# Kernel optimization log

Hardware: AMD Instinct MI355X
Metric: run time of the kernel (lower is better)

Reference implementation:

```python
import jax, jax.numpy as jnp
import numpy as np

B, N, H = 8, 1024, 1024
HEADS, DH = 16, 64  # H = HEADS * DH
LN_EPS = 1e-12


def setup_inputs() -> dict:
    key = jax.random.key(0)
    ks = jax.random.split(key, 8)
    s = 0.02
    return {
        "hidden_states": jax.random.normal(ks[0], (B, N, H), jnp.float32),
        "role_mask": jax.random.randint(ks[1], (B, N, N), 0, 2, jnp.int32),
        "conv_len": jax.random.randint(ks[2], (B,), 0, 160, jnp.int32),
        "Wq": jax.random.normal(ks[3], (H, H), jnp.float32) * s,
        "bq": jnp.zeros((H,), jnp.float32),
        "Wk": jax.random.normal(ks[4], (H, H), jnp.float32) * s,
        "bk": jnp.zeros((H,), jnp.float32),
        "Wv": jax.random.normal(ks[5], (H, H), jnp.float32) * s,
        "bv": jnp.zeros((H,), jnp.float32),
        "Wo": jax.random.normal(ks[6], (H, H), jnp.float32) * s,
        "bo": jnp.zeros((H,), jnp.float32),
        "gamma": jnp.ones((H,), jnp.float32),
        "beta": jnp.zeros((H,), jnp.float32),
    }


def _split_heads(x):
    b, n, h = x.shape
    return x.reshape(b, n, HEADS, DH).transpose(0, 2, 1, 3)  # [B,h,N,dh]


def reference(hidden_states, role_mask, conv_len, Wq, bq, Wk, bk, Wv, bv, Wo, bo, gamma, beta):
    q = _split_heads(hidden_states @ Wq + bq)
    k = _split_heads(hidden_states @ Wk + bk)
    v = _split_heads(hidden_states @ Wv + bv)

    scale = 1.0 / jnp.sqrt(jnp.asarray(DH, hidden_states.dtype))
    scores = jnp.einsum("bhqd,bhkd->bhqk", q, k) * scale  # [B,h,N,N]
    scores = jnp.where(role_mask[:, None, :, :] == 0, jnp.asarray(-1e9, scores.dtype), scores)
    probs = jax.nn.softmax(scores, axis=-1)  # dropout is identity in eval

    ctx = jnp.einsum("bhqk,bhkd->bhqd", probs, v)
    ctx = ctx.transpose(0, 2, 1, 3).reshape(hidden_states.shape)  # [B,N,H]

    # output projection + residual + LayerNorm (BERT-style, eps=1e-12)
    y = ctx @ Wo + bo + hidden_states
    mu = jnp.mean(y, axis=-1, keepdims=True)
    var = jnp.mean(jnp.square(y - mu), axis=-1, keepdims=True)
    context_layer = (y - mu) / jnp.sqrt(var + LN_EPS) * gamma + beta

    # state_type == 'user': rows 6*idx+2 (perspective) and 6*idx+3 (emotion)
    bidx = jnp.arange(context_layer.shape[0])
    base = 6 * conv_len
    perspective_taking = context_layer[bidx, base + 2]  # [B,H]
    high_emo_states = context_layer[bidx, base + 3]     # [B,H]
    return context_layer, high_emo_states, perspective_taking
```

## Files before the change

kernel.cpp:

```cpp
#include <hip/hip_runtime.h>
#include <math.h>

#define HN 1024
#define BB 8
#define NN 1024
#define NHEADS 16
#define DH 64
#define M_ROWS (BB * NN)

typedef __attribute__((ext_vector_type(8))) short short8;
typedef __attribute__((ext_vector_type(8))) unsigned short ushort8v;
typedef __attribute__((ext_vector_type(4))) float floatx4;

__device__ __forceinline__ unsigned short f2bf(float f) {
    unsigned int u = __builtin_bit_cast(unsigned int, f);
    u += 0x7fffu + ((u >> 16) & 1u);
    return (unsigned short)(u >> 16);
}

__device__ __forceinline__ void gload16(const unsigned short* g, unsigned short* l) {
    __builtin_amdgcn_global_load_lds(
        (const __attribute__((address_space(1))) void*)g,
        (__attribute__((address_space(3))) void*)l, 16, 0, 0);
}

__global__ __launch_bounds__(256)
void cvt_hs_k(const float* __restrict__ in, unsigned short* __restrict__ out)
{
    int i = (blockIdx.x * 256 + threadIdx.x) * 4;
    float4 v = *(const float4*)(in + i);
    ushort4 o;
    o.x = f2bf(v.x); o.y = f2bf(v.y); o.z = f2bf(v.z); o.w = f2bf(v.w);
    *(ushort4*)&out[i] = o;
}

__global__ __launch_bounds__(256)
void cvt_wT4_k(const float* __restrict__ W0, const float* __restrict__ W1,
               const float* __restrict__ W2, const float* __restrict__ W3,
               unsigned short* __restrict__ o0, unsigned short* __restrict__ o1,
               unsigned short* __restrict__ o2, unsigned short* __restrict__ o3)
{
    __shared__ float Ls[32][33];
    const int z = blockIdx.z;
    const float* W = z == 0 ? W0 : (z == 1 ? W1 : (z == 2 ? W2 : W3));
    unsigned short* out = z == 0 ? o0 : (z == 1 ? o1 : (z == 2 ? o2 : o3));
    const int t = threadIdx.x;
    const int k0 = blockIdx.x * 32, n0 = blockIdx.y * 32;
    const int r = t >> 3, c4 = (t & 7) * 4;
    float4 v = *(const float4*)(W + (size_t)(k0 + r) * HN + n0 + c4);
    Ls[r][c4 + 0] = v.x; Ls[r][c4 + 1] = v.y;
    Ls[r][c4 + 2] = v.z; Ls[r][c4 + 3] = v.w;
    __syncthreads();
    ushort4 o;
    o.x = f2bf(Ls[c4 + 0][r]); o.y = f2bf(Ls[c4 + 1][r]);
    o.z = f2bf(Ls[c4 + 2][r]); o.w = f2bf(Ls[c4 + 3][r]);
    *(ushort4*)&out[(size_t)(n0 + r) * HN + k0 + c4] = o;
}

__global__ __launch_bounds__(256)
void mfma_gemm_k(const unsigned short* __restrict__ A,
                 const unsigned short* __restrict__ Bt,
                 const float* __restrict__ b0p, const float* __restrict__ b1p,
                 const float* __restrict__ b2p,
                 const float* __restrict__ resid,
                 unsigned short* __restrict__ Qb, unsigned short* __restrict__ Kb,
                 unsigned short* __restrict__ Vtb, float* __restrict__ Yb,
                 int mode)
{
    __shared__ unsigned short smem[128 * 136];
    unsigned short* As = smem;
    unsigned short* Bs = smem + 4096;

    const int tid  = threadIdx.x;
    const int wave = tid >> 6, lane = tid & 63;
    const int quad = lane >> 4, n16 = lane & 15;
    const int wm = wave >> 1, wn = wave & 1;
    const int row0 = blockIdx.y * 128;
    const int n0   = blockIdx.x * 128;

    floatx4 acc[4][4];
    #pragma unroll
    for (int mi = 0; mi < 4; ++mi)
        #pragma unroll
        for (int ni = 0; ni < 4; ++ni)
            acc[mi][ni] = (floatx4){0.f, 0.f, 0.f, 0.f};

    const unsigned short* ga = A  + (size_t)(row0 + wave * 32 + (lane >> 2)) * 1024 + (lane & 3) * 8;
    const unsigned short* gb = Bt + (size_t)(n0  + wave * 32 + (lane >> 2)) * 1024 + (lane & 3) * 8;

    for (int k0 = 0; k0 < 1024; k0 += 32) {
        gload16(ga,             As + wave * 1024);
        gload16(ga + 16 * 1024, As + wave * 1024 + 512);
        gload16(gb,             Bs + wave * 1024);
        gload16(gb + 16 * 1024, Bs + wave * 1024 + 512);
        ga += 32; gb += 32;
        __syncthreads();

        short8 a[4], b[4];
        #pragma unroll
        for (int mi = 0; mi < 4; ++mi)
            a[mi] = *(const short8*)&As[(wm * 64 + mi * 16 + n16) * 32 + quad * 8];
        #pragma unroll
        for (int ni = 0; ni < 4; ++ni)
            b[ni] = *(const short8*)&Bs[(wn * 64 + ni * 16 + n16) * 32 + quad * 8];
        #pragma unroll
        for (int mi = 0; mi < 4; ++mi)
            #pragma unroll
            for (int ni = 0; ni < 4; ++ni)
                acc[mi][ni] = __builtin_amdgcn_mfma_f32_16x16x32_bf16(
                    a[mi], b[ni], acc[mi][ni], 0, 0, 0);
        __syncthreads();
    }

    if (mode == 0) {
        const int sel = n0 >> 10;
        const int c0  = n0 & 1023;
        const float* bias = sel == 0 ? b0p : (sel == 1 ? b1p : b2p);
        float bvv[4];
        #pragma unroll
        for (int ni = 0; ni < 4; ++ni)
            bvv[ni] = bias[c0 + wn * 64 + ni * 16 + n16];

        #pragma unroll
        for (int mi = 0; mi < 4; ++mi)
            #pragma unroll
            for (int ni = 0; ni < 4; ++ni)
                #pragma unroll
                for (int r = 0; r < 4; ++r)
                    smem[(wm * 64 + mi * 16 + quad * 4 + r) * 136 +
                         wn * 64 + ni * 16 + n16] = f2bf(acc[mi][ni][r] + bvv[ni]);
        __syncthreads();

        if (sel < 2) {
            unsigned short* outb = sel == 0 ? Qb : Kb;
            #pragma unroll
            for (int i = 0; i < 8; ++i) {
                int c = i * 256 + tid;
                int r = c >> 4;
                int colc = (c & 15) * 8;
                ushort8v v = *(const ushort8v*)&smem[r * 136 + colc];
                int row = row0 + r, bb = row >> 10, nn = row & 1023;
                int gc = c0 + colc, head = gc >> 6, d = gc & 63;
                *(ushort8v*)&outb[(((size_t)bb * NHEADS + head) * NN + nn) * DH + d] = v;
            }
        } else {
            #pragma unroll
            for (int i = 0; i < 8; ++i) {
                int c = i * 256 + tid;
                int dcol = c >> 4;
                int nnc = (c & 15) * 8;
                ushort8v v;
                #pragma unroll
                for (int j = 0; j < 8; ++j)
                    v[j] = smem[(nnc + j) * 136 + dcol];
                int gc = c0 + dcol, head = gc >> 6, d = gc & 63;
                int row = row0 + nnc, bb = row >> 10, nn = row & 1023;
                *(ushort8v*)&Vtb[(((size_t)bb * NHEADS + head) * DH + d) * NN + nn] = v;
            }
        }
    } else {
        float bvv[4];
        #pragma unroll
        for (int ni = 0; ni < 4; ++ni)
            bvv[ni] = b0p[n0 + wn * 64 + ni * 16 + n16];
        #pragma unroll
        for (int mi = 0; mi < 4; ++mi)
            #pragma unroll
            for (int r = 0; r < 4; ++r) {
                int row = row0 + wm * 64 + mi * 16 + quad * 4 + r;
                const float* rr = resid + (size_t)row * HN;
                float* yr = Yb + (size_t)row * HN;
                #pragma unroll
                for (int ni = 0; ni < 4; ++ni) {
                    int col = n0 + wn * 64 + ni * 16 + n16;
                    yr[col] = acc[mi][ni][r] + bvv[ni] + rr[col];
                }
            }
    }
}

__global__ __launch_bounds__(256)
void attn_mfma_k(const unsigned short* __restrict__ Q,
                 const unsigned short* __restrict__ K,
                 const unsigned short* __restrict__ Vt,
                 const int* __restrict__ mask,
                 unsigned short* __restrict__ ctx)
{
    __shared__ unsigned short KsB[2 * 4096];
    __shared__ unsigned short VsB[2 * 4096];
    __shared__ unsigned short PsB[4 * 1024];

    const int tid  = threadIdx.x;
    const int wave = tid >> 6, lane = tid & 63;
    const int quad = lane >> 4, n16 = lane & 15;
    const int sw   = n16 & 7;
    const int q0 = blockIdx.x << 6;
    const int h  = blockIdx.y, b = blockIdx.z;
    const int bh = b * NHEADS + h;
    const int qw = q0 + wave * 16;
    const float SC = 0.125f * 1.44269504088896340736f;

    const unsigned short* qp = Q + ((size_t)bh * NN + qw + n16) * DH;
    short8 aq0 = *(const short8*)(qp + quad * 8);
    short8 aq1 = *(const short8*)(qp + 32 + quad * 8);

    floatx4 O[4];
    #pragma unroll
    for (int d4 = 0; d4 < 4; ++d4) O[d4] = (floatx4){0.f, 0.f, 0.f, 0.f};
    float lsum = 0.f;

    const unsigned short* Kg = K  + (size_t)bh * NN * DH;
    const unsigned short* Vg = Vt + (size_t)bh * DH * NN;

    const int r8 = lane >> 3, cs = (lane & 7) ^ r8;
    const unsigned short* kg0 = Kg + (size_t)(wave * 16 + r8) * DH + cs * 8;
    const unsigned short* kg1 = kg0 + 8 * DH;
    const unsigned short* vg0 = Vg + (size_t)(wave * 16 + r8) * NN + cs * 8;
    const unsigned short* vg1 = vg0 + 8 * NN;
    unsigned short* lk = KsB + wave * 1024;
    unsigned short* lv = VsB + wave * 1024;
    unsigned short* Pw = PsB + wave * 1024;

    const int* mp = mask + ((size_t)b * NN + qw + n16) * NN + quad * 4;

    gload16(kg0, lk);       gload16(kg1, lk + 512);
    gload16(vg0, lv);       gload16(vg1, lv + 512);

    for (int t = 0; t < 16; ++t) {
        __syncthreads();
        const int cur = t & 1;
        if (t < 15) {
            const int nxt = cur ^ 1;
            kg0 += 4096; kg1 += 4096; vg0 += 64; vg1 += 64;
            gload16(kg0, lk + nxt * 4096); gload16(kg1, lk + nxt * 4096 + 512);
            gload16(vg0, lv + nxt * 4096); gload16(vg1, lv + nxt * 4096 + 512);
        }
        const unsigned short* Kc = KsB + cur * 4096;
        const unsigned short* Vc = VsB + cur * 4096;
        const int kbase = t * 64;

        #pragma unroll
        for (int kt = 0; kt < 4; ++kt) {
            const unsigned short* kr = Kc + (kt * 16 + n16) * 64;
            short8 kf0 = *(const short8*)&kr[(quad ^ sw) * 8];
            short8 kf1 = *(const short8*)&kr[((quad + 4) ^ sw) * 8];
            floatx4 s = (floatx4){0.f, 0.f, 0.f, 0.f};
            s = __builtin_amdgcn_mfma_f32_16x16x32_bf16(kf0, aq0, s, 0, 0, 0);
            s = __builtin_amdgcn_mfma_f32_16x16x32_bf16(kf1, aq1, s, 0, 0, 0);

            int4 m4 = *(const int4*)(mp + kbase + kt * 16);
            float p0 = m4.x ? exp2f(s[0] * SC) : 0.f;
            float p1 = m4.y ? exp2f(s[1] * SC) : 0.f;
            float p2 = m4.z ? exp2f(s[2] * SC) : 0.f;
            float p3 = m4.w ? exp2f(s[3] * SC) : 0.f;
            lsum += (p0 + p1) + (p2 + p3);
            ushort4 pk;
            pk.x = f2bf(p0); pk.y = f2bf(p1); pk.z = f2bf(p2); pk.w = f2bf(p3);
            *(ushort4*)&Pw[n16 * 64 + ((2 * kt + (quad >> 1)) ^ sw) * 8 +
                           (quad & 1) * 4] = pk;
        }

        #pragma unroll
        for (int c = 0; c < 2; ++c) {
            const int cc = ((c << 2) + quad) ^ sw;
            short8 pa = *(const short8*)&Pw[n16 * 64 + cc * 8];
            #pragma unroll
            for (int d4 = 0; d4 < 4; ++d4) {
                short8 vb = *(const short8*)&Vc[(d4 * 16 + n16) * 64 + cc * 8];
                O[d4] = __builtin_amdgcn_mfma_f32_16x16x32_bf16(pa, vb, O[d4], 0, 0, 0);
            }
        }
    }

    float ltot = lsum;
    ltot += __shfl_xor(ltot, 16);
    ltot += __shfl_xor(ltot, 32);
    float inv[4];
    #pragma unroll
    for (int r = 0; r < 4; ++r)
        inv[r] = 1.0f / __shfl(ltot, quad * 4 + r);

    unsigned short* cp = ctx + ((size_t)b * NN + qw + quad * 4) * HN + h * DH + n16;
    #pragma unroll
    for (int d4 = 0; d4 < 4; ++d4)
        #pragma unroll
        for (int r = 0; r < 4; ++r)
            cp[(size_t)r * HN + d4 * 16] = f2bf(O[d4][r] * inv[r]);
}

__global__ __launch_bounds__(256)
void ln_ext_k(const float* __restrict__ y, const float* __restrict__ gamma,
              const float* __restrict__ beta, const int* __restrict__ conv_len,
              float* __restrict__ out, float* __restrict__ he, float* __restrict__ pt)
{
    const int row = blockIdx.x;
    const int t = threadIdx.x;
    float4 v = ((const float4*)(y + (size_t)row * HN))[t];
    float s  = v.x + v.y + v.z + v.w;
    float s2 = v.x * v.x + v.y * v.y + v.z * v.z + v.w * v.w;
    #pragma unroll
    for (int off = 32; off > 0; off >>= 1) {
        s  += __shfl_down(s, off);
        s2 += __shfl_down(s2, off);
    }
    __shared__ float ws1[4], ws2[4];
    __shared__ float smu, sinv;
    if ((t & 63) == 0) { ws1[t >> 6] = s; ws2[t >> 6] = s2; }
    __syncthreads();
    if (t == 0) {
        float ts  = ws1[0] + ws1[1] + ws1[2] + ws1[3];
        float ts2 = ws2[0] + ws2[1] + ws2[2] + ws2[3];
        float mu  = ts * (1.0f / 1024.0f);
        float var = ts2 * (1.0f / 1024.0f) - mu * mu;
        smu  = mu;
        sinv = 1.0f / sqrtf(var + 1e-12f);
    }
    __syncthreads();
    const float mu = smu, inv = sinv;
    float4 g = ((const float4*)gamma)[t];
    float4 be = ((const float4*)beta)[t];
    float4 o;
    o.x = (v.x - mu) * inv * g.x + be.x;
    o.y = (v.y - mu) * inv * g.y + be.y;
    o.z = (v.z - mu) * inv * g.z + be.z;
    o.w = (v.w - mu) * inv * g.w + be.w;
    ((float4*)(out + (size_t)row * HN))[t] = o;

    const int b = row >> 10, n = row & 1023;
    const int base = 6 * conv_len[b];
    if (n == base + 3) ((float4*)(he + (size_t)b * HN))[t] = o;
    if (n == base + 2) ((float4*)(pt + (size_t)b * HN))[t] = o;
}

extern "C" void kernel_launch(void* const* d_in, const int* in_sizes, int n_in,
                              void* d_out, int out_size, void* d_ws, size_t ws_size,
                              hipStream_t stream)
{
    const float* hs    = (const float*)d_in[0];
    const int*   mask  = (const int*)d_in[1];
    const int*   clen  = (const int*)d_in[2];
    const float* Wq    = (const float*)d_in[3];
    const float* bq    = (const float*)d_in[4];
    const float* Wk    = (const float*)d_in[5];
    const float* bk    = (const float*)d_in[6];
    const float* Wv    = (const float*)d_in[7];
    const float* bv    = (const float*)d_in[8];
    const float* Wo    = (const float*)d_in[9];
    const float* bo    = (const float*)d_in[10];
    const float* gamma = (const float*)d_in[11];
    const float* beta  = (const float*)d_in[12];
    float* out = (float*)d_out;

    unsigned short* Ab  = (unsigned short*)d_ws;
    unsigned short* Wt3 = Ab  + (size_t)M_ROWS * HN;
    unsigned short* Wot = Wt3 + (size_t)3 * HN * HN;
    unsigned short* Qb  = Wot + (size_t)HN * HN;
    unsigned short* Kb  = Qb  + (size_t)M_ROWS * HN;
    unsigned short* Vtb = Kb  + (size_t)M_ROWS * HN;
    unsigned short* Ctx = Vtb + (size_t)M_ROWS * HN;
    float*          Yb  = (float*)Qb;

    dim3 gb(256);

    hipLaunchKernelGGL(cvt_hs_k, dim3((size_t)M_ROWS * HN / 1024), gb, 0, stream, hs, Ab);
    hipLaunchKernelGGL(cvt_wT4_k, dim3(32, 32, 4), gb, 0, stream,
                       Wq, Wk, Wv, Wo,
                       Wt3, Wt3 + (size_t)HN * HN, Wt3 + (size_t)2 * HN * HN, Wot);

    hipLaunchKernelGGL(mfma_gemm_k, dim3(24, 64), gb, 0, stream,
                       Ab, Wt3, bq, bk, bv, (const float*)nullptr,
                       Qb, Kb, Vtb, (float*)nullptr, 0);

    hipLaunchKernelGGL(attn_mfma_k, dim3(NN / 64, NHEADS, BB), gb, 0, stream,
                       Qb, Kb, Vtb, mask, Ctx);

    hipLaunchKernelGGL(mfma_gemm_k, dim3(8, 64), gb, 0, stream,
                       Ctx, Wot, bo, (const float*)nullptr, (const float*)nullptr, hs,
                       (unsigned short*)nullptr, (unsigned short*)nullptr,
                       (unsigned short*)nullptr, Yb, 1);

    float* he = out + (size_t)BB * NN * HN;
    float* pt = he + BB * HN;
    hipLaunchKernelGGL(ln_ext_k, dim3(M_ROWS), gb, 0, stream, Yb, gamma, beta, clen,
                       out, he, pt);
}
```

Before: 384.9 us.

## Keep attention probabilities in registers and process two query tiles per wave

The attention kernel now gives each wave 32 query rows (two 16-row subtiles), so every K and V fragment read from LDS feeds twice as many MFMAs, and the grid along the query axis is halved. The probability tile no longer goes through an LDS scratch buffer. The K tile is loaded in a permuted row order so that the score MFMA output layout already matches the B-operand layout of the PV MFMA, letting the packed bf16 probabilities be used straight from registers. Output stores are vectorised. The cost is higher register pressure, fewer blocks in flight, and a more intricate index mapping.

After: 389.8 us. About the same (+1.3%).

```diff
diff --git a/kernel.cpp b/kernel.cpp
--- a/kernel.cpp
+++ b/kernel.cpp
@@ -11,11 +11,16 @@
 typedef __attribute__((ext_vector_type(8))) short short8;
 typedef __attribute__((ext_vector_type(8))) unsigned short ushort8v;
 typedef __attribute__((ext_vector_type(4))) float floatx4;
+typedef __attribute__((ext_vector_type(4))) unsigned int uint4v;
 
 __device__ __forceinline__ unsigned short f2bf(float f) {
     unsigned int u = __builtin_bit_cast(unsigned int, f);
     u += 0x7fffu + ((u >> 16) & 1u);
     return (unsigned short)(u >> 16);
+}
+
+__device__ __forceinline__ unsigned int pack2bf(float a, float b) {
+    return (unsigned int)f2bf(a) | ((unsigned int)f2bf(b) << 16);
 }
 
 __device__ __forceinline__ void gload16(const unsigned short* g, unsigned short* l) {
@@ -188,43 +193,51 @@
 {
     __shared__ unsigned short KsB[2 * 4096];
     __shared__ unsigned short VsB[2 * 4096];
-    __shared__ unsigned short PsB[4 * 1024];
 
     const int tid  = threadIdx.x;
     const int wave = tid >> 6, lane = tid & 63;
     const int quad = lane >> 4, n16 = lane & 15;
     const int sw   = n16 & 7;
-    const int q0 = blockIdx.x << 6;
+    const int q0 = blockIdx.x << 7;
     const int h  = blockIdx.y, b = blockIdx.z;
     const int bh = b * NHEADS + h;
-    const int qw = q0 + wave * 16;
+    const int qw = q0 + wave * 32;
     const float SC = 0.125f * 1.44269504088896340736f;
 
-    const unsigned short* qp = Q + ((size_t)bh * NN + qw + n16) * DH;
-    short8 aq0 = *(const short8*)(qp + quad * 8);
-    short8 aq1 = *(const short8*)(qp + 32 + quad * 8);
-
-    floatx4 O[4];
+    short8 aq[2][2];
     #pragma unroll
-    for (int d4 = 0; d4 < 4; ++d4) O[d4] = (floatx4){0.f, 0.f, 0.f, 0.f};
-    float lsum = 0.f;
+    for (int qh = 0; qh < 2; ++qh) {
+        const unsigned short* qp = Q + ((size_t)bh * NN + qw + qh * 16 + n16) * DH;
+        aq[qh][0] = *(const short8*)(qp + quad * 8);
+        aq[qh][1] = *(const short8*)(qp + 32 + quad * 8);
+    }
+
+    floatx4 O[2][4];
+    #pragma unroll
+    for (int qh = 0; qh < 2; ++qh)
+        #pragma unroll
+        for (int d4 = 0; d4 < 4; ++d4)
+            O[qh][d4] = (floatx4){0.f, 0.f, 0.f, 0.f};
+    float lsum[2] = {0.f, 0.f};
 
     const unsigned short* Kg = K  + (size_t)bh * NN * DH;
     const unsigned short* Vg = Vt + (size_t)bh * DH * NN;
 
-    const int r8 = lane >> 3, cs = (lane & 7) ^ r8;
-    const unsigned short* kg0 = Kg + (size_t)(wave * 16 + r8) * DH + cs * 8;
-    const unsigned short* kg1 = kg0 + 8 * DH;
+    const int r8 = lane >> 3;
+    const int cs = (lane & 7) ^ (r8 & 7);
+    const int gk0 = ((wave >> 1) << 5) + ((r8 >> 2) << 3) + ((wave & 1) << 2) + (r8 & 3);
+    const unsigned short* kg0 = Kg + (size_t)gk0 * DH + cs * 8;
+    const unsigned short* kg1 = kg0 + 16 * DH;
     const unsigned short* vg0 = Vg + (size_t)(wave * 16 + r8) * NN + cs * 8;
     const unsigned short* vg1 = vg0 + 8 * NN;
     unsigned short* lk = KsB + wave * 1024;
     unsigned short* lv = VsB + wave * 1024;
-    unsigned short* Pw = PsB + wave * 1024;
-
-    const int* mp = mask + ((size_t)b * NN + qw + n16) * NN + quad * 4;
-
-    gload16(kg0, lk);       gload16(kg1, lk + 512);
-    gload16(vg0, lv);       gload16(vg1, lv + 512);
+
+    const int* mp0 = mask + ((size_t)b * NN + qw + n16) * NN + quad * 8;
+    const int* mp1 = mp0 + 16 * NN;
+
+    gload16(kg0, lk);  gload16(kg1, lk + 512);
+    gload16(vg0, lv);  gload16(vg1, lv + 512);
 
     for (int t = 0; t < 16; ++t) {
         __syncthreads();
@@ -239,53 +252,64 @@
         const unsigned short* Vc = VsB + cur * 4096;
         const int kbase = t * 64;
 
+        unsigned int pk[2][8];
         #pragma unroll
         for (int kt = 0; kt < 4; ++kt) {
             const unsigned short* kr = Kc + (kt * 16 + n16) * 64;
             short8 kf0 = *(const short8*)&kr[(quad ^ sw) * 8];
             short8 kf1 = *(const short8*)&kr[((quad + 4) ^ sw) * 8];
-            floatx4 s = (floatx4){0.f, 0.f, 0.f, 0.f};
-            s = __builtin_amdgcn_mfma_f32_16x16x32_bf16(kf0, aq0, s, 0, 0, 0);
-            s = __builtin_amdgcn_mfma_f32_16x16x32_bf16(kf1, aq1, s, 0, 0, 0);
-
-            int4 m4 = *(const int4*)(mp + kbase + kt * 16);
-            float p0 = m4.x ? exp2f(s[0] * SC) : 0.f;
-            float p1 = m4.y ? exp2f(s[1] * SC) : 0.f;
-            float p2 = m4.z ? exp2f(s[2] * SC) : 0.f;
-            float p3 = m4.w ? exp2f(s[3] * SC) : 0.f;
-            lsum += (p0 + p1) + (p2 + p3);
-            ushort4 pk;
-            pk.x = f2bf(p0); pk.y = f2bf(p1); pk.z = f2bf(p2); pk.w = f2bf(p3);
-            *(ushort4*)&Pw[n16 * 64 + ((2 * kt + (quad >> 1)) ^ sw) * 8 +
-                           (quad & 1) * 4] = pk;
-        }
-
-        #pragma unroll
-        for (int c = 0; c < 2; ++c) {
-            const int cc = ((c << 2) + quad) ^ sw;
-            short8 pa = *(const short8*)&Pw[n16 * 64 + cc * 8];
-            #pragma unroll
-            for (int d4 = 0; d4 < 4; ++d4) {
-                short8 vb = *(const short8*)&Vc[(d4 * 16 + n16) * 64 + cc * 8];
-                O[d4] = __builtin_amdgcn_mfma_f32_16x16x32_bf16(pa, vb, O[d4], 0, 0, 0);
+            const int moff = kbase + ((kt >> 1) << 5) + ((kt & 1) << 2);
+            #pragma unroll
+            for (int qh = 0; qh < 2; ++qh) {
+                floatx4 s = (floatx4){0.f, 0.f, 0.f, 0.f};
+                s = __builtin_amdgcn_mfma_f32_16x16x32_bf16(kf0, aq[qh][0], s, 0, 0, 0);
+                s = __builtin_amdgcn_mfma_f32_16x16x32_bf16(kf1, aq[qh][1], s, 0, 0, 0);
+                int4 m4 = *(const int4*)((qh ? mp1 : mp0) + moff);
+                float p0 = m4.x ? exp2f(s[0] * SC) : 0.f;
+                float p1 = m4.y ? exp2f(s[1] * SC) : 0.f;
+                float p2 = m4.z ? exp2f(s[2] * SC) : 0.f;
+                float p3 = m4.w ? exp2f(s[3] * SC) : 0.f;
+                lsum[qh] += (p0 + p1) + (p2 + p3);
+                pk[qh][kt * 2]     = pack2bf(p0, p1);
+                pk[qh][kt * 2 + 1] = pack2bf(p2, p3);
             }
         }
-    }
-
-    float ltot = lsum;
-    ltot += __shfl_xor(ltot, 16);
-    ltot += __shfl_xor(ltot, 32);
-    float inv[4];
+
+        #pragma unroll
+        for (int c = 0; c < 2; ++c) {
+            short8 vb[4];
+            #pragma unroll
+            for (int d4 = 0; d4 < 4; ++d4)
+                vb[d4] = *(const short8*)&Vc[(d4 * 16 + n16) * 64 +
+                                             ((4 * c + quad) ^ sw) * 8];
+            #pragma unroll
+            for (int qh = 0; qh < 2; ++qh) {
+                uint4v u = {pk[qh][c * 4], pk[qh][c * 4 + 1],
+                            pk[qh][c * 4 + 2], pk[qh][c * 4 + 3]};
+                short8 pb = __builtin_bit_cast(short8, u);
+                #pragma unroll
+                for (int d4 = 0; d4 < 4; ++d4)
+                    O[qh][d4] = __builtin_amdgcn_mfma_f32_16x16x32_bf16(
+                        vb[d4], pb, O[qh][d4], 0, 0, 0);
+            }
+        }
+    }
+
     #pragma unroll
-    for (int r = 0; r < 4; ++r)
-        inv[r] = 1.0f / __shfl(ltot, quad * 4 + r);
-
-    unsigned short* cp = ctx + ((size_t)b * NN + qw + quad * 4) * HN + h * DH + n16;
-    #pragma unroll
-    for (int d4 = 0; d4 < 4; ++d4)
-        #pragma unroll
-        for (int r = 0; r < 4; ++r)
-            cp[(size_t)r * HN + d4 * 16] = f2bf(O[d4][r] * inv[r]);
+    for (int qh = 0; qh < 2; ++qh) {
+        float ltot = lsum[qh];
+        ltot += __shfl_xor(ltot, 16);
+        ltot += __shfl_xor(ltot, 32);
+        const float inv = 1.0f / ltot;
+        unsigned short* cp = ctx + ((size_t)b * NN + qw + qh * 16 + n16) * HN
+                             + h * DH + quad * 4;
+        #pragma unroll
+        for (int d4 = 0; d4 < 4; ++d4) {
+            unsigned int u01 = pack2bf(O[qh][d4][0] * inv, O[qh][d4][1] * inv);
+            unsigned int u23 = pack2bf(O[qh][d4][2] * inv, O[qh][d4][3] * inv);
+            *(uint2*)(cp + d4 * 16) = (uint2){u01, u23};
+        }
+    }
 }
 
 __global__ __launch_bounds__(256)
@@ -371,7 +395,7 @@
                        Ab, Wt3, bq, bk, bv, (const float*)nullptr,
                        Qb, Kb, Vtb, (float*)nullptr, 0);
 
-    hipLaunchKernelGGL(attn_mfma_k, dim3(NN / 64, NHEADS, BB), gb, 0, stream,
+    hipLaunchKernelGGL(attn_mfma_k, dim3(NN / 128, NHEADS, BB), gb, 0, stream,
                        Qb, Kb, Vtb, mask, Ctx);
 
     hipLaunchKernelGGL(mfma_gemm_k, dim3(8, 64), gb, 0, stream,
```
